# Kernel tuning notes

Measured on AMD Instinct MI355X. Metric: run time of the kernel, lower is better.

Reference implementation:

```python
import jax, jax.numpy as jnp
import numpy as np

B, S, D = 4, 4096, 64
TEMPERATURE = 8.0  # sqrt(64), matching Dense(64) projections in source


def setup_inputs() -> dict:
    key = jax.random.key(0)
    kq, kk, kv = jax.random.split(key, 3)
    q = jax.random.normal(kq, (B, S, D), dtype=jnp.float32)
    k = jax.random.normal(kk, (B, S, D), dtype=jnp.float32)
    v = jax.random.normal(kv, (B, S, D), dtype=jnp.float32)
    return {"q": q, "k": k, "v": v}


def reference(q, k, v):
    # attn = softmax(QK^T / temperature); dropout is identity at inference
    scores = jnp.einsum("bqd,bkd->bqk", q, k) / TEMPERATURE  # [B,S,S]
    attn = jax.nn.softmax(scores, axis=-1)
    out = jnp.einsum("bqk,bkd->bqd", attn, v)  # [B,S,D]
    return (out, attn)
```

## Files before the change

### kernel.cpp

```cpp
#include <hip/hip_runtime.h>
#include <cstddef>

namespace {
constexpr int kB = 4;
constexpr int kS = 4096;
constexpr int kD = 64;
constexpr float kC = 0.18033688011112042f;

typedef float  f32x4  __attribute__((ext_vector_type(4)));
typedef __bf16 bf16x8 __attribute__((ext_vector_type(8)));
typedef short  s16x2  __attribute__((ext_vector_type(2)));
typedef short  s16x4  __attribute__((ext_vector_type(4)));
typedef short  s16x8  __attribute__((ext_vector_type(8)));
typedef int    i32x4  __attribute__((ext_vector_type(4)));

constexpr size_t kWsQ = (size_t)kB * kS * kD;
constexpr size_t kWsNeed = 3 * kWsQ * sizeof(short);
}

__device__ __forceinline__ s16x2 pack_bf16(float a, float b) {
    __bf16 ha = (__bf16)a, hb = (__bf16)b;
    s16x2 r;
    r.x = __builtin_bit_cast(short, ha);
    r.y = __builtin_bit_cast(short, hb);
    return r;
}

__global__ __launch_bounds__(256)
void prepass_kernel(const float* __restrict__ q, const float* __restrict__ k,
                    const float* __restrict__ v, short* __restrict__ qb,
                    short* __restrict__ kb, short* __restrict__ vt)
{
    __shared__ float lt[64][65];
    const int bid = blockIdx.x, tid = threadIdx.x;
    if (bid < 512) {
        const float* src = (bid < 256) ? q : k;
        short* dst = (bid < 256) ? qb : kb;
        const int base = (bid & 255) * 4096;
        #pragma unroll
        for (int c = 0; c < 4; ++c) {
            const int idx = base + c * 1024 + tid * 4;
            float4 f = *(const float4*)(src + idx);
            s16x4 o = __builtin_shufflevector(pack_bf16(f.x, f.y), pack_bf16(f.z, f.w), 0, 1, 2, 3);
            *(s16x4*)(dst + idx) = o;
        }
    } else {
        const int vb = bid - 512;
        const int b = vb >> 6, j0 = (vb & 63) * 64;
        const int r = tid >> 2, seg = tid & 3;
        const float* vrow = v + ((size_t)(b * kS) + j0 + r) * kD + seg * 16;
        #pragma unroll
        for (int u = 0; u < 4; ++u) {
            float4 f = *(const float4*)(vrow + 4 * u);
            lt[r][seg * 16 + 4 * u + 0] = f.x;
            lt[r][seg * 16 + 4 * u + 1] = f.y;
            lt[r][seg * 16 + 4 * u + 2] = f.z;
            lt[r][seg * 16 + 4 * u + 3] = f.w;
        }
        __syncthreads();
        const int d = r, js = seg * 16;
        short* drow = vt + ((size_t)(b * kD) + d) * kS + j0 + js;
        #pragma unroll
        for (int w = 0; w < 4; ++w) {
            s16x4 o = __builtin_shufflevector(
                pack_bf16(lt[js + 4 * w + 0][d], lt[js + 4 * w + 1][d]),
                pack_bf16(lt[js + 4 * w + 2][d], lt[js + 4 * w + 3][d]), 0, 1, 2, 3);
            *(s16x4*)(drow + 4 * w) = o;
        }
    }
}

__global__ __launch_bounds__(512, 8)
void attn_mfma_kernel(const short* __restrict__ qb, const short* __restrict__ kb,
                      const short* __restrict__ vt, float* __restrict__ outg,
                      float* __restrict__ attng)
{
    __shared__ __align__(16) float lds_out[7][16][68];
    __shared__ float lds_rs[8][16];
    __shared__ float lds_linv[16];

    const int swz = (blockIdx.x & 7) * 128 + (blockIdx.x >> 3);
    const int b  = swz >> 8;
    const int i0 = (swz & 255) * 16;
    const int lane = threadIdx.x & 63;
    const int wave = threadIdx.x >> 6;
    const int t = lane & 15;
    const int q = lane >> 4;

    const short* Qb = qb + ((size_t)(b * kS) + i0) * kD;
    const short* Kb = kb + (size_t)(b * kS) * kD;
    const short* Vt = vt + (size_t)b * kD * kS;

    const bf16x8 qf0 = *(const bf16x8*)(Qb + t * kD + 8 * q);
    const bf16x8 qf1 = *(const bf16x8*)(Qb + t * kD + 32 + 8 * q);

    const int jbeg = wave * (kS / 8);
    const int jend = jbeg + (kS / 8);
    const int sA = t + 32 * (q & 1);

    f32x4 oacc[4];
    #pragma unroll
    for (int dt = 0; dt < 4; ++dt) oacc[dt] = (f32x4){0.f, 0.f, 0.f, 0.f};
    float rs = 0.f;

    for (int j0 = jbeg; j0 < jend; j0 += 32) {
        int p0 = 0, p1 = 0, p2 = 0, p3 = 0;
        #pragma unroll
        for (int h = 0; h < 2; ++h) {
            const short* p = Kb + (size_t)(j0 + 16 * h + t) * kD + 8 * q;
            const bf16x8 ka0 = *(const bf16x8*)p;
            const bf16x8 ka1 = *(const bf16x8*)(p + 32);
            f32x4 acc = (f32x4){0.f, 0.f, 0.f, 0.f};
            acc = __builtin_amdgcn_mfma_f32_16x16x32_bf16(ka0, qf0, acc, 0, 0, 0);
            acc = __builtin_amdgcn_mfma_f32_16x16x32_bf16(ka1, qf1, acc, 0, 0, 0);
            const float e0 = __builtin_amdgcn_exp2f(acc[0] * kC);
            const float e1 = __builtin_amdgcn_exp2f(acc[1] * kC);
            const float e2 = __builtin_amdgcn_exp2f(acc[2] * kC);
            const float e3 = __builtin_amdgcn_exp2f(acc[3] * kC);
            rs += (e0 + e1) + (e2 + e3);
            const int d0 = __builtin_bit_cast(int, pack_bf16(e0, e1));
            const int d1 = __builtin_bit_cast(int, pack_bf16(e2, e3));
            const int a0 = __shfl(d0, sA);
            const int a1 = __shfl(d1, sA);
            const int b0 = __shfl(d0, sA + 16);
            const int b1 = __shfl(d1, sA + 16);
            if ((q >> 1) == h) { p0 = a0; p1 = a1; p2 = b0; p3 = b1; }
        }
        const i32x4 pi = (i32x4){p0, p1, p2, p3};
        const bf16x8 pa = __builtin_bit_cast(bf16x8, pi);

        #pragma unroll
        for (int dt = 0; dt < 4; ++dt) {
            const bf16x8 vb = *(const bf16x8*)(Vt + (size_t)(16 * dt + t) * kS + j0 + 8 * q);
            oacc[dt] = __builtin_amdgcn_mfma_f32_16x16x32_bf16(pa, vb, oacc[dt], 0, 0, 0);
        }
    }

    rs += __shfl_xor(rs, 16);
    rs += __shfl_xor(rs, 32);

    if (lane < 16) lds_rs[wave][t] = rs;
    if (wave > 0) {
        #pragma unroll
        for (int dt = 0; dt < 4; ++dt)
            #pragma unroll
            for (int r = 0; r < 4; ++r)
                lds_out[wave - 1][4 * q + r][16 * dt + t] = oacc[dt][r];
    }
    __syncthreads();
    if (wave == 0) {
        #pragma unroll
        for (int w = 0; w < 7; ++w)
            #pragma unroll
            for (int dt = 0; dt < 4; ++dt)
                #pragma unroll
                for (int r = 0; r < 4; ++r)
                    oacc[dt][r] += lds_out[w][4 * q + r][16 * dt + t];
        float tot = 0.f;
        #pragma unroll
        for (int w = 0; w < 8; ++w) tot += lds_rs[w][t];
        if (lane < 16) lds_linv[t] = 1.0f / tot;
    }
    __syncthreads();

    if (wave == 0) {
        #pragma unroll
        for (int r = 0; r < 4; ++r) {
            const float li = lds_linv[4 * q + r];
            float* orow = outg + ((size_t)(b * kS) + i0 + 4 * q + r) * kD + t;
            #pragma unroll
            for (int dt = 0; dt < 4; ++dt)
                orow[16 * dt] = oacc[dt][r] * li;
        }
    }

    const float l0 = lds_linv[4 * q + 0];
    const float l1 = lds_linv[4 * q + 1];
    const float l2 = lds_linv[4 * q + 2];
    const float l3 = lds_linv[4 * q + 3];

    float* a0 = attng + ((size_t)(b * kS) + i0 + 4 * q + 0) * kS + t;
    float* a1 = attng + ((size_t)(b * kS) + i0 + 4 * q + 1) * kS + t;
    float* a2 = attng + ((size_t)(b * kS) + i0 + 4 * q + 2) * kS + t;
    float* a3 = attng + ((size_t)(b * kS) + i0 + 4 * q + 3) * kS + t;

    #pragma unroll 2
    for (int j0 = jbeg; j0 < jend; j0 += 16) {
        const short* p = Kb + (size_t)(j0 + t) * kD + 8 * q;
        const bf16x8 ka0 = *(const bf16x8*)p;
        const bf16x8 ka1 = *(const bf16x8*)(p + 32);
        f32x4 acc = (f32x4){0.f, 0.f, 0.f, 0.f};
        acc = __builtin_amdgcn_mfma_f32_16x16x32_bf16(qf0, ka0, acc, 0, 0, 0);
        acc = __builtin_amdgcn_mfma_f32_16x16x32_bf16(qf1, ka1, acc, 0, 0, 0);
        const float o0 = __builtin_amdgcn_exp2f(acc[0] * kC) * l0;
        const float o1 = __builtin_amdgcn_exp2f(acc[1] * kC) * l1;
        const float o2 = __builtin_amdgcn_exp2f(acc[2] * kC) * l2;
        const float o3 = __builtin_amdgcn_exp2f(acc[3] * kC) * l3;
        a0[j0] = o0;
        a1[j0] = o1;
        a2[j0] = o2;
        a3[j0] = o3;
    }
}

namespace fb {
constexpr int QT = 64, JT = 64;
constexpr float kScale = 0.125f;
constexpr int LP = kD + 4;
}
__global__ __launch_bounds__(256, 1)
void attn_fp32_kernel(const float* __restrict__ qg, const float* __restrict__ kg,
                      const float* __restrict__ vg, float* __restrict__ outg,
                      float* __restrict__ attng)
{
    using namespace fb;
    __shared__ float qs[QT][LP];
    __shared__ float ks[JT][LP];
    __shared__ float es[QT][JT + 4];
    __shared__ float red[QT][17];
    __shared__ float linv[QT];
    const int tid = threadIdx.x;
    const int tx = tid & 15, ty = tid >> 4;
    const int b = blockIdx.x >> 6, qt = blockIdx.x & 63, i0 = qt * QT;
    const float* qbp = qg + ((size_t)b * kS + i0) * kD;
    const float* kbase = kg + (size_t)b * kS * kD;
    const float* vbase = vg + (size_t)b * kS * kD;
    {
        const int r = tid >> 4, c4 = (tid & 15) * 4;
        #pragma unroll
        for (int m = 0; m < 4; ++m)
            *(float4*)&qs[r + 16 * m][c4] = *(const float4*)(qbp + (r + 16 * m) * kD + c4);
    }
    float oacc[4][4]; float rsv[4];
    #pragma unroll
    for (int r = 0; r < 4; ++r) { rsv[r] = 0.f; for (int c = 0; c < 4; ++c) oacc[r][c] = 0.f; }
    for (int jt = 0; jt < kS / JT; ++jt) {
        const float* kt = kbase + (size_t)(jt * JT) * kD;
        const int r = tid >> 4, c4 = (tid & 15) * 4;
        #pragma unroll
        for (int m = 0; m < 4; ++m)
            *(float4*)&ks[r + 16 * m][c4] = *(const float4*)(kt + (r + 16 * m) * kD + c4);
        __syncthreads();
        float acc[4][4] = {{0.f}};
        #pragma unroll
        for (int d4 = 0; d4 < kD / 4; ++d4) {
            float4 qa[4], kav[4];
            #pragma unroll
            for (int r2 = 0; r2 < 4; ++r2) qa[r2] = *(const float4*)&qs[ty * 4 + r2][d4 * 4];
            #pragma unroll
            for (int c = 0; c < 4; ++c) kav[c] = *(const float4*)&ks[tx * 4 + c][d4 * 4];
            #pragma unroll
            for (int r2 = 0; r2 < 4; ++r2)
                #pragma unroll
                for (int c = 0; c < 4; ++c)
                    acc[r2][c] += qa[r2].x * kav[c].x + qa[r2].y * kav[c].y
                                + qa[r2].z * kav[c].z + qa[r2].w * kav[c].w;
        }
        #pragma unroll
        for (int r2 = 0; r2 < 4; ++r2) {
            float4 e4;
            e4.x = __expf(acc[r2][0] * kScale); e4.y = __expf(acc[r2][1] * kScale);
            e4.z = __expf(acc[r2][2] * kScale); e4.w = __expf(acc[r2][3] * kScale);
            rsv[r2] += (e4.x + e4.y) + (e4.z + e4.w);
            *(float4*)&es[ty * 4 + r2][tx * 4] = e4;
        }
        __syncthreads();
        const float* vt2 = vbase + (size_t)(jt * JT) * kD;
        #pragma unroll 4
        for (int j4 = 0; j4 < JT / 4; ++j4) {
            float4 vv[4], ea[4];
            #pragma unroll
            for (int n = 0; n < 4; ++n) vv[n] = *(const float4*)(vt2 + (size_t)(j4 * 4 + n) * kD + tx * 4);
            #pragma unroll
            for (int r2 = 0; r2 < 4; ++r2) ea[r2] = *(const float4*)&es[ty * 4 + r2][j4 * 4];
            #pragma unroll
            for (int r2 = 0; r2 < 4; ++r2) {
                oacc[r2][0] += ea[r2].x * vv[0].x + ea[r2].y * vv[1].x + ea[r2].z * vv[2].x + ea[r2].w * vv[3].x;
                oacc[r2][1] += ea[r2].x * vv[0].y + ea[r2].y * vv[1].y + ea[r2].z * vv[2].y + ea[r2].w * vv[3].y;
                oacc[r2][2] += ea[r2].x * vv[0].z + ea[r2].y * vv[1].z + ea[r2].z * vv[2].z + ea[r2].w * vv[3].z;
                oacc[r2][3] += ea[r2].x * vv[0].w + ea[r2].y * vv[1].w + ea[r2].z * vv[2].w + ea[r2].w * vv[3].w;
            }
        }
        __syncthreads();
    }
    #pragma unroll
    for (int r = 0; r < 4; ++r) red[ty * 4 + r][tx] = rsv[r];
    __syncthreads();
    if (tid < QT) {
        float s = 0.f;
        #pragma unroll
        for (int t2 = 0; t2 < 16; ++t2) s += red[tid][t2];
        linv[tid] = 1.0f / s;
    }
    __syncthreads();
    {
        float* ob = outg + ((size_t)b * kS + i0) * kD;
        #pragma unroll
        for (int r = 0; r < 4; ++r) {
            const int i = ty * 4 + r; const float li = linv[i];
            float4 o4; o4.x = oacc[r][0] * li; o4.y = oacc[r][1] * li;
            o4.z = oacc[r][2] * li; o4.w = oacc[r][3] * li;
            *(float4*)(ob + (size_t)i * kD + tx * 4) = o4;
        }
    }
    float* ab = attng + ((size_t)b * kS + i0) * kS;
    for (int jt = 0; jt < kS / JT; ++jt) {
        const float* kt = kbase + (size_t)(jt * JT) * kD;
        const int r = tid >> 4, c4 = (tid & 15) * 4;
        #pragma unroll
        for (int m = 0; m < 4; ++m)
            *(float4*)&ks[r + 16 * m][c4] = *(const float4*)(kt + (r + 16 * m) * kD + c4);
        __syncthreads();
        float acc[4][4] = {{0.f}};
        #pragma unroll
        for (int d4 = 0; d4 < kD / 4; ++d4) {
            float4 qa[4], kav[4];
            #pragma unroll
            for (int r2 = 0; r2 < 4; ++r2) qa[r2] = *(const float4*)&qs[ty * 4 + r2][d4 * 4];
            #pragma unroll
            for (int c = 0; c < 4; ++c) kav[c] = *(const float4*)&ks[tx * 4 + c][d4 * 4];
            #pragma unroll
            for (int r2 = 0; r2 < 4; ++r2)
                #pragma unroll
                for (int c = 0; c < 4; ++c)
                    acc[r2][c] += qa[r2].x * kav[c].x + qa[r2].y * kav[c].y
                                + qa[r2].z * kav[c].z + qa[r2].w * kav[c].w;
        }
        #pragma unroll
        for (int r2 = 0; r2 < 4; ++r2) {
            const int i = ty * 4 + r2; const float li = linv[i];
            float4 e4;
            e4.x = __expf(acc[r2][0] * kScale) * li; e4.y = __expf(acc[r2][1] * kScale) * li;
            e4.z = __expf(acc[r2][2] * kScale) * li; e4.w = __expf(acc[r2][3] * kScale) * li;
            *(float4*)(ab + (size_t)i * kS + jt * JT + tx * 4) = e4;
        }
        __syncthreads();
    }
}

extern "C" void kernel_launch(void* const* d_in, const int* in_sizes, int n_in,
                              void* d_out, int out_size, void* d_ws, size_t ws_size,
                              hipStream_t stream) {
    const float* q = (const float*)d_in[0];
    const float* k = (const float*)d_in[1];
    const float* v = (const float*)d_in[2];
    float* out  = (float*)d_out;
    float* attn = out + (size_t)kB * kS * kD;

    if (ws_size >= kWsNeed) {
        short* qb = (short*)d_ws;
        short* kbp = qb + kWsQ;
        short* vt = kbp + kWsQ;
        prepass_kernel<<<dim3(768), 256, 0, stream>>>(q, k, v, qb, kbp, vt);
        attn_mfma_kernel<<<dim3(kB * (kS / 16)), 512, 0, stream>>>(qb, kbp, vt, out, attn);
    } else {
        attn_fp32_kernel<<<dim3(kB * (kS / 64)), 256, 0, stream>>>(q, k, v, out, attn);
    }
}
```

Before: 430.1 us.

## Stage attention probabilities in LDS for coalesced vectorized global stores

The second pass that recomputes QK^T and writes normalized probabilities now writes each 16x512 chunk into a shared LDS buffer (reusing the reduction scratch space). After a barrier, each wave writes two full rows with 16-byte vector stores instead of scattered 4-byte stores with stride kS. The goal is to cut the cost of the dominant 256MB attn write through better coalescing, at the price of two block barriers per chunk and extra LDS traffic. It also replaces the per-wave j-range loop with a chunked loop that covers all columns.

```diff
diff --git a/kernel.cpp b/kernel.cpp
--- a/kernel.cpp
+++ b/kernel.cpp
@@ -75,7 +75,8 @@
                       const short* __restrict__ vt, float* __restrict__ outg,
                       float* __restrict__ attng)
 {
-    __shared__ __align__(16) float lds_out[7][16][68];
+    constexpr int ST = 516;
+    __shared__ __align__(16) float pool[16 * ST];
     __shared__ float lds_rs[8][16];
     __shared__ float lds_linv[16];
 
@@ -145,7 +146,7 @@
         for (int dt = 0; dt < 4; ++dt)
             #pragma unroll
             for (int r = 0; r < 4; ++r)
-                lds_out[wave - 1][4 * q + r][16 * dt + t] = oacc[dt][r];
+                pool[((wave - 1) * 16 + 4 * q + r) * 68 + 16 * dt + t] = oacc[dt][r];
     }
     __syncthreads();
     if (wave == 0) {
@@ -155,7 +156,7 @@
             for (int dt = 0; dt < 4; ++dt)
                 #pragma unroll
                 for (int r = 0; r < 4; ++r)
-                    oacc[dt][r] += lds_out[w][4 * q + r][16 * dt + t];
+                    oacc[dt][r] += pool[(w * 16 + 4 * q + r) * 68 + 16 * dt + t];
         float tot = 0.f;
         #pragma unroll
         for (int w = 0; w < 8; ++w) tot += lds_rs[w][t];
@@ -179,27 +180,40 @@
     const float l2 = lds_linv[4 * q + 2];
     const float l3 = lds_linv[4 * q + 3];
 
-    float* a0 = attng + ((size_t)(b * kS) + i0 + 4 * q + 0) * kS + t;
-    float* a1 = attng + ((size_t)(b * kS) + i0 + 4 * q + 1) * kS + t;
-    float* a2 = attng + ((size_t)(b * kS) + i0 + 4 * q + 2) * kS + t;
-    float* a3 = attng + ((size_t)(b * kS) + i0 + 4 * q + 3) * kS + t;
-
-    #pragma unroll 2
-    for (int j0 = jbeg; j0 < jend; j0 += 16) {
-        const short* p = Kb + (size_t)(j0 + t) * kD + 8 * q;
-        const bf16x8 ka0 = *(const bf16x8*)p;
-        const bf16x8 ka1 = *(const bf16x8*)(p + 32);
-        f32x4 acc = (f32x4){0.f, 0.f, 0.f, 0.f};
-        acc = __builtin_amdgcn_mfma_f32_16x16x32_bf16(qf0, ka0, acc, 0, 0, 0);
-        acc = __builtin_amdgcn_mfma_f32_16x16x32_bf16(qf1, ka1, acc, 0, 0, 0);
-        const float o0 = __builtin_amdgcn_exp2f(acc[0] * kC) * l0;
-        const float o1 = __builtin_amdgcn_exp2f(acc[1] * kC) * l1;
-        const float o2 = __builtin_amdgcn_exp2f(acc[2] * kC) * l2;
-        const float o3 = __builtin_amdgcn_exp2f(acc[3] * kC) * l3;
-        a0[j0] = o0;
-        a1[j0] = o1;
-        a2[j0] = o2;
-        a3[j0] = o3;
+    const int row0 = 2 * wave;
+    float* grow0 = attng + ((size_t)(b * kS) + i0 + row0 + 0) * kS;
+    float* grow1 = attng + ((size_t)(b * kS) + i0 + row0 + 1) * kS;
+
+    for (int c = 0; c < 8; ++c) {
+        const int jc = c * 512;
+        const int jw = jc + wave * 64;
+        #pragma unroll
+        for (int m = 0; m < 4; ++m) {
+            const int j0 = jw + 16 * m;
+            const short* p = Kb + (size_t)(j0 + t) * kD + 8 * q;
+            const bf16x8 ka0 = *(const bf16x8*)p;
+            const bf16x8 ka1 = *(const bf16x8*)(p + 32);
+            f32x4 acc = (f32x4){0.f, 0.f, 0.f, 0.f};
+            acc = __builtin_amdgcn_mfma_f32_16x16x32_bf16(qf0, ka0, acc, 0, 0, 0);
+            acc = __builtin_amdgcn_mfma_f32_16x16x32_bf16(qf1, ka1, acc, 0, 0, 0);
+            const int col = wave * 64 + 16 * m + t;
+            pool[(4 * q + 0) * ST + col] = __builtin_amdgcn_exp2f(acc[0] * kC) * l0;
+            pool[(4 * q + 1) * ST + col] = __builtin_amdgcn_exp2f(acc[1] * kC) * l1;
+            pool[(4 * q + 2) * ST + col] = __builtin_amdgcn_exp2f(acc[2] * kC) * l2;
+            pool[(4 * q + 3) * ST + col] = __builtin_amdgcn_exp2f(acc[3] * kC) * l3;
+        }
+        __syncthreads();
+        {
+            const f32x4 v00 = *(const f32x4*)&pool[(row0 + 0) * ST + 0   + lane * 4];
+            const f32x4 v01 = *(const f32x4*)&pool[(row0 + 0) * ST + 256 + lane * 4];
+            *(f32x4*)(grow0 + jc + 0   + lane * 4) = v00;
+            *(f32x4*)(grow0 + jc + 256 + lane * 4) = v01;
+            const f32x4 v10 = *(const f32x4*)&pool[(row0 + 1) * ST + 0   + lane * 4];
+            const f32x4 v11 = *(const f32x4*)&pool[(row0 + 1) * ST + 256 + lane * 4];
+            *(f32x4*)(grow1 + jc + 0   + lane * 4) = v10;
+            *(f32x4*)(grow1 + jc + 256 + lane * 4) = v11;
+        }
+        __syncthreads();
     }
 }
 
```

New measurement: 415.6 us. -3.4%, faster.
